# Kernel optimization log

Hardware: AMD Instinct MI355X
Metric: run time of the kernel (lower is better)

The kernel has to match this reference:

```python
import jax, jax.numpy as jnp
import numpy as np

EMB = 768
HEADS = 12
B, N = 32, 1024


def setup_inputs() -> dict:
    key = jax.random.key(0)
    ks = jax.random.split(key, 7)
    s = 1.0 / np.sqrt(EMB)
    return {
        "x": jax.random.normal(ks[0], (B, N, EMB), dtype=jnp.float32),
        "Wq": jax.random.normal(ks[1], (EMB, EMB), dtype=jnp.float32) * s,
        "bq": jnp.zeros((EMB,), dtype=jnp.float32),
        "Wk": jax.random.normal(ks[2], (EMB, EMB), dtype=jnp.float32) * s,
        "bk": jnp.zeros((EMB,), dtype=jnp.float32),
        "Wv": jax.random.normal(ks[3], (EMB, EMB), dtype=jnp.float32) * s,
        "bv": jnp.zeros((EMB,), dtype=jnp.float32),
    }


def reference(x, Wq, bq, Wk, bk, Wv, bv):
    b, n, _ = x.shape
    h = HEADS
    e = EMB // h  # head dim
    # project and split heads: b n (h e) -> b h n e
    def split(t):
        return t.reshape(b, n, h, e).transpose(0, 2, 1, 3)
    q = split(x @ Wq + bq)
    k = split(x @ Wk + bk)
    v = split(x @ Wv + bv)
    # NOTE: scale is 1/sqrt(num_head), as in the original module
    wei = jnp.einsum('bhie,bhje->bhij', q, k) / jnp.sqrt(jnp.float32(h))
    # NOTE: softmax over dim=2 = query axis i (non-standard)
    wei = jax.nn.softmax(wei, axis=2)
    # dropout is identity in eval mode
    out = jnp.einsum('bhij,bhje->bhie', wei, v)
    return out.transpose(0, 2, 1, 3).reshape(b, n, h * e)
```

## Files before the change

### kernel.cpp

```cpp
#include <hip/hip_runtime.h>

#define EMB 768
#define NH 12
#define HD 64
#define BB 32
#define NN 1024
#define QSCALE 0.41647025f

typedef _Float16 h8 __attribute__((ext_vector_type(8)));
typedef _Float16 h4 __attribute__((ext_vector_type(4)));
typedef _Float16 h2 __attribute__((ext_vector_type(2)));
typedef float f4 __attribute__((ext_vector_type(4)));

static __device__ __forceinline__ f4 mfma16(h8 a, h8 b, f4 c) {
  return __builtin_amdgcn_mfma_f32_16x16x32_f16(a, b, c, 0, 0, 0);
}

static __device__ __forceinline__ h2 cvt_pk(float a, float b) {
  return __builtin_bit_cast(h2, __builtin_amdgcn_cvt_pkrtz(a, b));
}

static __device__ __forceinline__ float exp2a(float x) {
#if __has_builtin(__builtin_amdgcn_exp2f)
  return __builtin_amdgcn_exp2f(x);
#else
  float r;
  asm("v_exp_f32 %0, %1\n\ts_nop 1" : "=v"(r) : "v"(x));
  return r;
#endif
}

__global__ __launch_bounds__(256) void k_cvt(const float* __restrict__ X,
                                             _Float16* __restrict__ Xh, int n4) {
  int i = blockIdx.x * 256 + threadIdx.x;
  if (i >= n4) return;
  float4 v = ((const float4*)X)[i];
  h4 o = {(_Float16)v.x, (_Float16)v.y, (_Float16)v.z, (_Float16)v.w};
  ((h4*)Xh)[i] = o;
}

__global__ __launch_bounds__(256) void k_wt(const float* __restrict__ W0,
                                            const float* __restrict__ W1,
                                            const float* __restrict__ W2,
                                            _Float16* __restrict__ Wt) {
  const float* W = blockIdx.z == 0 ? W0 : (blockIdx.z == 1 ? W1 : W2);
  _Float16* dst = Wt + (size_t)blockIdx.z * EMB * EMB;
  __shared__ float tile[64][65];
  const int t = threadIdx.x;
  const int r0 = blockIdx.y * 64, c0 = blockIdx.x * 64;
  const int r = t >> 4, c4 = (t & 15) * 4;
#pragma unroll
  for (int i = 0; i < 4; ++i) {
    const float4 v = *(const float4*)&W[(size_t)(r0 + r + 16 * i) * EMB + c0 + c4];
    tile[r + 16 * i][c4 + 0] = v.x; tile[r + 16 * i][c4 + 1] = v.y;
    tile[r + 16 * i][c4 + 2] = v.z; tile[r + 16 * i][c4 + 3] = v.w;
  }
  __syncthreads();
  const int cc = t >> 2, rr = (t & 3) * 16;
#pragma unroll
  for (int half = 0; half < 2; ++half) {
    h8 o;
#pragma unroll
    for (int j = 0; j < 8; ++j) o[j] = (_Float16)tile[rr + half * 8 + j][cc];
    *(h8*)&dst[(size_t)(c0 + cc) * EMB + r0 + rr + half * 8] = o;
  }
}

__global__ __launch_bounds__(256) void k_proj(const _Float16* __restrict__ Xh,
                                              const _Float16* __restrict__ Wt,
                                              const float* __restrict__ bias,
                                              _Float16* __restrict__ Out, float scale) {
  __shared__ _Float16 As[128][40];
  __shared__ _Float16 Bs[128][40];
  const int t = threadIdx.x;
  const int w = t >> 6, l = t & 63;
  const int wm = w >> 1, wn = w & 1;
  const int m0 = blockIdx.x * 128, n0 = blockIdx.y * 128;
  f4 acc[4][4];
#pragma unroll
  for (int mf = 0; mf < 4; ++mf)
#pragma unroll
    for (int nf = 0; nf < 4; ++nf) acc[mf][nf] = f4{0.f, 0.f, 0.f, 0.f};

  const int srow = t >> 2, sc = (t & 3) * 8;
  for (int k0 = 0; k0 < EMB; k0 += 32) {
#pragma unroll
    for (int i = 0; i < 2; ++i) {
      *(h8*)&As[srow + 64 * i][sc] = *(const h8*)&Xh[(size_t)(m0 + srow + 64 * i) * EMB + k0 + sc];
      *(h8*)&Bs[srow + 64 * i][sc] = *(const h8*)&Wt[(size_t)(n0 + srow + 64 * i) * EMB + k0 + sc];
    }
    __syncthreads();
    h8 af[4], bf[4];
#pragma unroll
    for (int mf = 0; mf < 4; ++mf) af[mf] = *(const h8*)&As[wm * 64 + mf * 16 + (l & 15)][(l >> 4) * 8];
#pragma unroll
    for (int nf = 0; nf < 4; ++nf) bf[nf] = *(const h8*)&Bs[wn * 64 + nf * 16 + (l & 15)][(l >> 4) * 8];
#pragma unroll
    for (int mf = 0; mf < 4; ++mf)
#pragma unroll
      for (int nf = 0; nf < 4; ++nf) acc[mf][nf] = mfma16(af[mf], bf[nf], acc[mf][nf]);
    __syncthreads();
  }
#pragma unroll
  for (int nf = 0; nf < 4; ++nf) {
    const int C = n0 + wn * 64 + nf * 16 + (l & 15);
    const float bvv = bias[C];
    const int h = C >> 6, e = C & 63;
#pragma unroll
    for (int mf = 0; mf < 4; ++mf) {
#pragma unroll
      for (int r = 0; r < 4; ++r) {
        const int R = m0 + wm * 64 + mf * 16 + (l >> 4) * 4 + r;
        const int b = R >> 10, tok = R & 1023;
        Out[((size_t)(b * NH + h) * NN + tok) * HD + e] = (_Float16)((acc[mf][nf][r] + bvv) * scale);
      }
    }
  }
}

__global__ __launch_bounds__(256) void k_stats(const _Float16* __restrict__ Q,
                                               const _Float16* __restrict__ K,
                                               float* __restrict__ Lg, float* __restrict__ MT) {
  const int bh = blockIdx.x * 48 + (blockIdx.y >> 3);
  const int jt = blockIdx.y & 7;
  const int j0 = jt * 128;
  __shared__ _Float16 Ks[128][64];
  __shared__ _Float16 Qs[128][64];
  __shared__ float Lj[128];
  __shared__ float reds[2][128];
  __shared__ float MsSh;
  const _Float16* Qb = Q + (size_t)bh * NN * HD;
  const _Float16* Kb = K + (size_t)bh * NN * HD;
  const int t = threadIdx.x, w = t >> 6, l = t & 63;
  const int wi = w >> 1, wj = w & 1;
  const int p = l & 15, g = l >> 4;
  const int lr = t >> 3, tc = t & 7;
  char* ksb = (char*)&Ks[0][0];
  char* qsb = (char*)&Qs[0][0];
#pragma unroll
  for (int i = 0; i < 4; ++i)
    *(h8*)(ksb + ((lr + 32 * i) << 7) + ((tc ^ (lr & 7)) << 4)) =
        *(const h8*)&Kb[(size_t)(j0 + lr + 32 * i) * HD + tc * 8];
  if (t < 128) Lj[t] = 0.f;
  __syncthreads();

  for (int i0 = 0; i0 < NN; i0 += 128) {
#pragma unroll
    for (int i = 0; i < 4; ++i)
      *(h8*)(qsb + ((lr + 32 * i) << 7) + ((tc ^ (lr & 7)) << 4)) =
          *(const h8*)&Qb[(size_t)(i0 + lr + 32 * i) * HD + tc * 8];
    __syncthreads();
    f4 s[4][4];
#pragma unroll
    for (int mf = 0; mf < 4; ++mf)
#pragma unroll
      for (int nf = 0; nf < 4; ++nf) s[mf][nf] = f4{0.f, 0.f, 0.f, 0.f};
#pragma unroll
    for (int ks = 0; ks < 2; ++ks) {
      h8 af[4], bf[4];
#pragma unroll
      for (int mf = 0; mf < 4; ++mf)
        af[mf] = *(const h8*)(qsb + ((wi * 64 + mf * 16 + p) << 7) + ((((ks << 2) | g) ^ (p & 7)) << 4));
#pragma unroll
      for (int nf = 0; nf < 4; ++nf)
        bf[nf] = *(const h8*)(ksb + ((wj * 64 + nf * 16 + p) << 7) + ((((ks << 2) | g) ^ (p & 7)) << 4));
#pragma unroll
      for (int mf = 0; mf < 4; ++mf)
#pragma unroll
        for (int nf = 0; nf < 4; ++nf) s[mf][nf] = mfma16(af[mf], bf[nf], s[mf][nf]);
    }
#pragma unroll
    for (int nf = 0; nf < 4; ++nf) {
      float cs = 0.f;
#pragma unroll
      for (int mf = 0; mf < 4; ++mf)
#pragma unroll
        for (int r = 0; r < 4; ++r) cs += exp2a(s[mf][nf][r]);
      cs += __shfl_xor(cs, 16);
      cs += __shfl_xor(cs, 32);
      if (l < 16) reds[wi][wj * 64 + nf * 16 + l] = cs;
    }
    __syncthreads();
    if (t < 128) Lj[t] += reds[0][t] + reds[1][t];
    __syncthreads();
  }
  if (w == 0) {
    float mv = fmaxf(Lj[l], Lj[l + 64]);
#pragma unroll
    for (int d = 32; d; d >>= 1) mv = fmaxf(mv, __shfl_xor(mv, d));
    if (l == 0) { MsSh = __log2f(mv); MT[bh * 8 + jt] = MsSh; }
  }
  __syncthreads();
  const float msc = exp2a(-MsSh);
  if (t < 128) Lg[(size_t)bh * NN + j0 + t] = Lj[t] * msc;
}

__global__ __launch_bounds__(256) void k_vt(const _Float16* __restrict__ Vtmp,
                                            const float* __restrict__ Lg,
                                            _Float16* __restrict__ Vt) {
  const int bh = blockIdx.y, j0 = blockIdx.x * 64;
  __shared__ _Float16 tile[64][72];
  const _Float16* src = Vtmp + (size_t)bh * NN * HD;
  _Float16* dst = Vt + (size_t)bh * HD * NN;
  const int t = threadIdx.x;
  const int jr = t >> 3, e8 = (t & 7) * 8;
#pragma unroll
  for (int i = 0; i < 2; ++i) {
    const float inv = 1.0f / Lg[(size_t)bh * NN + j0 + jr + 32 * i];
    h8 v = *(const h8*)&src[(size_t)(j0 + jr + 32 * i) * HD + e8];
    h8 o;
#pragma unroll
    for (int j = 0; j < 8; ++j) o[j] = (_Float16)((float)v[j] * inv);
    *(h8*)&tile[jr + 32 * i][e8] = o;
  }
  __syncthreads();
  const int er = t >> 3, j8 = (t & 7) * 8;
#pragma unroll
  for (int i = 0; i < 2; ++i) {
    h8 o;
#pragma unroll
    for (int j = 0; j < 8; ++j) o[j] = tile[j8 + j][er + 32 * i];
    *(h8*)&dst[(size_t)(er + 32 * i) * NN + j0 + j8] = o;
  }
}

__global__ __launch_bounds__(256) void k_out(const _Float16* __restrict__ Q,
                                             const _Float16* __restrict__ K,
                                             const _Float16* __restrict__ Vt,
                                             const float* __restrict__ MT,
                                             float* __restrict__ Out) {
  const int bh = blockIdx.x * 48 + (blockIdx.y >> 2);
  const int i0 = (blockIdx.y & 3) * 256;
  const int b = bh / NH, h = bh % NH;
  __shared__ _Float16 Ks[2][32][64];
  __shared__ _Float16 Vts[2][64][32];
  __shared__ _Float16 Ps[4][2][32][32];
  const _Float16* Qb = Q + (size_t)bh * NN * HD;
  const _Float16* Kb = K + (size_t)bh * NN * HD;
  const _Float16* Vb = Vt + (size_t)bh * HD * NN;
  const int t = threadIdx.x, w = t >> 6, l = t & 63;
  const int p = l & 15, g = l >> 4;
  char* psb[2] = {(char*)&Ps[w][0][0][0], (char*)&Ps[w][1][0][0]};

  h8 bq[2][2][2];
#pragma unroll
  for (int it = 0; it < 2; ++it)
#pragma unroll
    for (int f = 0; f < 2; ++f)
#pragma unroll
      for (int ks = 0; ks < 2; ++ks)
        bq[it][f][ks] = *(const h8*)&Qb[(size_t)(i0 + it * 128 + w * 32 + f * 16 + p) * HD + ks * 32 + g * 8];

  f4 oacc[2][4][2];
#pragma unroll
  for (int it = 0; it < 2; ++it)
#pragma unroll
    for (int ef = 0; ef < 4; ++ef)
#pragma unroll
      for (int f = 0; f < 2; ++f) oacc[it][ef][f] = f4{0.f, 0.f, 0.f, 0.f};

  const int kr = t >> 3, kc = t & 7;
  const int vr = t >> 2, vc = t & 3;

  h8 kreg = *(const h8*)&Kb[(size_t)kr * HD + kc * 8];
  h8 vreg = *(const h8*)&Vb[(size_t)vr * NN + vc * 8];
  *(h8*)((char*)&Ks[0][0][0] + (kr << 7) + ((kc ^ (kr & 7)) << 4)) = kreg;
  *(h8*)((char*)&Vts[0][0][0] + (vr << 6) + ((vc ^ ((vr >> 1) & 3)) << 4)) = vreg;

  for (int jt4 = 0; jt4 < 8; ++jt4) {
    const float Mstar = MT[bh * 8 + jt4];
#pragma unroll
    for (int u = 0; u < 4; ++u) {
      const int jt = jt4 * 4 + u;
      const int cur = u & 1;
      char* ksb = (char*)&Ks[cur][0][0];
      char* vsb = (char*)&Vts[cur][0][0];
      __syncthreads();
      if (jt + 1 < 32) {
        const int j0n = (jt + 1) * 32;
        kreg = *(const h8*)&Kb[(size_t)(j0n + kr) * HD + kc * 8];
        vreg = *(const h8*)&Vb[(size_t)vr * NN + j0n + vc * 8];
      }

      h8 ak[2][2], av[4];
#pragma unroll
      for (int ks = 0; ks < 2; ++ks)
#pragma unroll
        for (int jf = 0; jf < 2; ++jf)
          ak[ks][jf] = *(const h8*)(ksb + ((jf * 16 + p) << 7) + ((((ks << 2) | g) ^ (p & 7)) << 4));
#pragma unroll
      for (int ef = 0; ef < 4; ++ef)
        av[ef] = *(const h8*)(vsb + ((ef * 16 + p) << 6) + ((g ^ ((p >> 1) & 3)) << 4));

#pragma unroll
      for (int it = 0; it < 2; ++it) {
        f4 s[2][2];
#pragma unroll
        for (int f = 0; f < 2; ++f)
#pragma unroll
          for (int jf = 0; jf < 2; ++jf) s[f][jf] = f4{-Mstar, -Mstar, -Mstar, -Mstar};
#pragma unroll
        for (int ks = 0; ks < 2; ++ks)
#pragma unroll
          for (int f = 0; f < 2; ++f)
#pragma unroll
            for (int jf = 0; jf < 2; ++jf) s[f][jf] = mfma16(ak[ks][jf], bq[it][f][ks], s[f][jf]);
#pragma unroll
        for (int f = 0; f < 2; ++f)
#pragma unroll
          for (int jf = 0; jf < 2; ++jf) {
            const f4 sv = s[f][jf];
            h2 lo = cvt_pk(exp2a(sv[0]), exp2a(sv[1]));
            h2 hi = cvt_pk(exp2a(sv[2]), exp2a(sv[3]));
            h4 pw; pw[0] = lo[0]; pw[1] = lo[1]; pw[2] = hi[0]; pw[3] = hi[1];
            *(h4*)(psb[it] + ((f * 16 + p) << 6) +
                   (((2 * jf + (g >> 1)) ^ ((p >> 1) & 3)) << 4) + ((g & 1) << 3)) = pw;
          }
      }
      asm volatile("s_waitcnt lgkmcnt(0)" ::: "memory");
      __builtin_amdgcn_sched_barrier(0);

#pragma unroll
      for (int it = 0; it < 2; ++it) {
        h8 bp[2];
#pragma unroll
        for (int f = 0; f < 2; ++f)
          bp[f] = *(const h8*)(psb[it] + ((f * 16 + p) << 6) + ((g ^ ((p >> 1) & 3)) << 4));
#pragma unroll
        for (int ef = 0; ef < 4; ++ef)
#pragma unroll
          for (int f = 0; f < 2; ++f) oacc[it][ef][f] = mfma16(av[ef], bp[f], oacc[it][ef][f]);
      }

      if (jt + 1 < 32) {
        *(h8*)((char*)&Ks[cur ^ 1][0][0] + (kr << 7) + ((kc ^ (kr & 7)) << 4)) = kreg;
        *(h8*)((char*)&Vts[cur ^ 1][0][0] + (vr << 6) + ((vc ^ ((vr >> 1) & 3)) << 4)) = vreg;
      }
    }
  }

#pragma unroll
  for (int it = 0; it < 2; ++it) {
#pragma unroll
    for (int f = 0; f < 2; ++f) {
      const int i = i0 + it * 128 + w * 32 + f * 16 + p;
#pragma unroll
      for (int ef = 0; ef < 4; ++ef) {
        float4 o4 = {oacc[it][ef][f][0], oacc[it][ef][f][1], oacc[it][ef][f][2], oacc[it][ef][f][3]};
        *(float4*)&Out[((size_t)b * NN + i) * EMB + h * HD + ef * 16 + 4 * g] = o4;
      }
    }
  }
}

extern "C" void kernel_launch(void* const* d_in, const int* in_sizes, int n_in,
                              void* d_out, int out_size, void* d_ws, size_t ws_size,
                              hipStream_t stream) {
  const float* X  = (const float*)d_in[0];
  const float* Wq = (const float*)d_in[1];
  const float* bq = (const float*)d_in[2];
  const float* Wk = (const float*)d_in[3];
  const float* bk = (const float*)d_in[4];
  const float* Wv = (const float*)d_in[5];
  const float* bv = (const float*)d_in[6];

  char* ws = (char*)d_ws;
  _Float16* Qw = (_Float16*)(ws);
  _Float16* Kw = (_Float16*)(ws + 50331648);
  _Float16* Vt = (_Float16*)(ws + 100663296);
  _Float16* Wt = (_Float16*)(ws + 150994944);
  float* Lg    = (float*)(ws + 154533888);
  float* MT    = (float*)(ws + 156106752);

  _Float16* Xh   = (_Float16*)d_out;
  _Float16* Vtmp = (_Float16*)((char*)d_out + 50331648);
  float* Out = (float*)d_out;

  k_cvt<<<dim3(6291456 / 256), 256, 0, stream>>>(X, Xh, 6291456);
  k_wt<<<dim3(12, 12, 3), 256, 0, stream>>>(Wq, Wk, Wv, Wt);
  k_proj<<<dim3(256, 6), 256, 0, stream>>>(Xh, Wt,           bq, Qw,   QSCALE);
  k_proj<<<dim3(256, 6), 256, 0, stream>>>(Xh, Wt + 589824,  bk, Kw,   1.0f);
  k_proj<<<dim3(256, 6), 256, 0, stream>>>(Xh, Wt + 1179648, bv, Vtmp, 1.0f);
  k_stats<<<dim3(8, 384), 256, 0, stream>>>(Qw, Kw, Lg, MT);
  k_vt<<<dim3(16, 384), 256, 0, stream>>>(Vtmp, Lg, Vt);
  k_out<<<dim3(8, 192), 256, 0, stream>>>(Qw, Kw, Vt, MT, Out);
}
```

Baseline: 447.0 us.

## Fuse QKV projections into one GEMM with async LDS double-buffering

Replaces the three separate projection launches with one kernel over a 2304-wide concatenated weight, so each block picks its Q/K/V output, bias and scale from its column tile. K-tiles grow to 64 and are loaded straight into LDS with global_load_lds into a double buffer using an XOR swizzle. This is meant to overlap global loads with MFMA work, avoid LDS bank conflicts, cut launch overhead and improve X tile reuse through L2 across the fused N dimension. LDS use rises to 64KB per block, which may lower occupancy.

```diff
diff --git a/kernel.cpp b/kernel.cpp
--- a/kernel.cpp
+++ b/kernel.cpp
@@ -28,6 +28,12 @@
   asm("v_exp_f32 %0, %1\n\ts_nop 1" : "=v"(r) : "v"(x));
   return r;
 #endif
+}
+
+static __device__ __forceinline__ void gload16(const _Float16* g, _Float16* lds) {
+  __builtin_amdgcn_global_load_lds(
+      (const __attribute__((address_space(1))) void*)g,
+      (__attribute__((address_space(3))) void*)lds, 16, 0, 0);
 }
 
 __global__ __launch_bounds__(256) void k_cvt(const float* __restrict__ X,
@@ -66,53 +72,90 @@
   }
 }
 
-__global__ __launch_bounds__(256) void k_proj(const _Float16* __restrict__ Xh,
-                                              const _Float16* __restrict__ Wt,
-                                              const float* __restrict__ bias,
-                                              _Float16* __restrict__ Out, float scale) {
-  __shared__ _Float16 As[128][40];
-  __shared__ _Float16 Bs[128][40];
+__global__ __launch_bounds__(256) void k_projf(const _Float16* __restrict__ Xh,
+                                               const _Float16* __restrict__ Wt,
+                                               const float* __restrict__ bq,
+                                               const float* __restrict__ bk,
+                                               const float* __restrict__ bv,
+                                               _Float16* __restrict__ Qw,
+                                               _Float16* __restrict__ Kw,
+                                               _Float16* __restrict__ Vtmp) {
+  __shared__ _Float16 As[2][128 * 64];
+  __shared__ _Float16 Bs[2][128 * 64];
   const int t = threadIdx.x;
   const int w = t >> 6, l = t & 63;
   const int wm = w >> 1, wn = w & 1;
-  const int m0 = blockIdx.x * 128, n0 = blockIdx.y * 128;
+  const int p = l & 15, g = l >> 4;
+  const int by = blockIdx.x;
+  const int m0 = blockIdx.y * 128;
+  const int n0 = by * 128;
+
   f4 acc[4][4];
 #pragma unroll
   for (int mf = 0; mf < 4; ++mf)
 #pragma unroll
     for (int nf = 0; nf < 4; ++nf) acc[mf][nf] = f4{0.f, 0.f, 0.f, 0.f};
 
-  const int srow = t >> 2, sc = (t & 3) * 8;
-  for (int k0 = 0; k0 < EMB; k0 += 32) {
-#pragma unroll
-    for (int i = 0; i < 2; ++i) {
-      *(h8*)&As[srow + 64 * i][sc] = *(const h8*)&Xh[(size_t)(m0 + srow + 64 * i) * EMB + k0 + sc];
-      *(h8*)&Bs[srow + 64 * i][sc] = *(const h8*)&Wt[(size_t)(n0 + srow + 64 * i) * EMB + k0 + sc];
+  const int lrow = l >> 3, lch = (l & 7) ^ (l >> 3);
+
+#define STAGE(buf, k0)                                                            \
+  {                                                                               \
+    _Float16* ab = &As[buf][0];                                                   \
+    _Float16* bb = &Bs[buf][0];                                                   \
+    _Pragma("unroll") for (int i = 0; i < 4; ++i) {                               \
+      const int seg = (w << 2) | i;                                               \
+      const int grow = (seg << 3) | lrow;                                         \
+      gload16(Xh + (size_t)(m0 + grow) * EMB + (k0) + lch * 8, ab + seg * 512);   \
+      gload16(Wt + (size_t)(n0 + grow) * EMB + (k0) + lch * 8, bb + seg * 512);   \
+    }                                                                             \
+  }
+
+  STAGE(0, 0)
+  __syncthreads();
+
+  int cur = 0;
+  for (int kt = 0; kt < 12; ++kt) {
+    if (kt + 1 < 12) STAGE(cur ^ 1, (kt + 1) * 64)
+    const char* asb = (const char*)&As[cur][0];
+    const char* bsb = (const char*)&Bs[cur][0];
+#pragma unroll
+    for (int ks = 0; ks < 2; ++ks) {
+      h8 af[4], bf[4];
+#pragma unroll
+      for (int mf = 0; mf < 4; ++mf)
+        af[mf] = *(const h8*)(asb + ((wm * 64 + mf * 16 + p) << 7) +
+                              ((((ks << 2) | g) ^ (p & 7)) << 4));
+#pragma unroll
+      for (int nf = 0; nf < 4; ++nf)
+        bf[nf] = *(const h8*)(bsb + ((wn * 64 + nf * 16 + p) << 7) +
+                              ((((ks << 2) | g) ^ (p & 7)) << 4));
+#pragma unroll
+      for (int mf = 0; mf < 4; ++mf)
+#pragma unroll
+        for (int nf = 0; nf < 4; ++nf) acc[mf][nf] = mfma16(af[mf], bf[nf], acc[mf][nf]);
     }
     __syncthreads();
-    h8 af[4], bf[4];
-#pragma unroll
-    for (int mf = 0; mf < 4; ++mf) af[mf] = *(const h8*)&As[wm * 64 + mf * 16 + (l & 15)][(l >> 4) * 8];
-#pragma unroll
-    for (int nf = 0; nf < 4; ++nf) bf[nf] = *(const h8*)&Bs[wn * 64 + nf * 16 + (l & 15)][(l >> 4) * 8];
-#pragma unroll
-    for (int mf = 0; mf < 4; ++mf)
-#pragma unroll
-      for (int nf = 0; nf < 4; ++nf) acc[mf][nf] = mfma16(af[mf], bf[nf], acc[mf][nf]);
-    __syncthreads();
-  }
+    cur ^= 1;
+  }
+#undef STAGE
+
+  const int z = by / 6;
+  const int nl0 = (by % 6) * 128;
+  const float* bias = z == 0 ? bq : (z == 1 ? bk : bv);
+  _Float16* Outz = z == 0 ? Qw : (z == 1 ? Kw : Vtmp);
+  const float scale = z == 0 ? QSCALE : 1.0f;
 #pragma unroll
   for (int nf = 0; nf < 4; ++nf) {
-    const int C = n0 + wn * 64 + nf * 16 + (l & 15);
+    const int C = nl0 + wn * 64 + nf * 16 + p;
     const float bvv = bias[C];
     const int h = C >> 6, e = C & 63;
 #pragma unroll
     for (int mf = 0; mf < 4; ++mf) {
 #pragma unroll
       for (int r = 0; r < 4; ++r) {
-        const int R = m0 + wm * 64 + mf * 16 + (l >> 4) * 4 + r;
+        const int R = m0 + wm * 64 + mf * 16 + g * 4 + r;
         const int b = R >> 10, tok = R & 1023;
-        Out[((size_t)(b * NH + h) * NN + tok) * HD + e] = (_Float16)((acc[mf][nf][r] + bvv) * scale);
+        Outz[((size_t)(b * NH + h) * NN + tok) * HD + e] = (_Float16)((acc[mf][nf][r] + bvv) * scale);
       }
     }
   }
@@ -378,9 +421,7 @@
 
   k_cvt<<<dim3(6291456 / 256), 256, 0, stream>>>(X, Xh, 6291456);
   k_wt<<<dim3(12, 12, 3), 256, 0, stream>>>(Wq, Wk, Wv, Wt);
-  k_proj<<<dim3(256, 6), 256, 0, stream>>>(Xh, Wt,           bq, Qw,   QSCALE);
-  k_proj<<<dim3(256, 6), 256, 0, stream>>>(Xh, Wt + 589824,  bk, Kw,   1.0f);
-  k_proj<<<dim3(256, 6), 256, 0, stream>>>(Xh, Wt + 1179648, bv, Vtmp, 1.0f);
+  k_projf<<<dim3(18, 256), 256, 0, stream>>>(Xh, Wt, bq, bk, bv, Qw, Kw, Vtmp);
   k_stats<<<dim3(8, 384), 256, 0, stream>>>(Qw, Kw, Lg, MT);
   k_vt<<<dim3(16, 384), 256, 0, stream>>>(Vtmp, Lg, Vt);
   k_out<<<dim3(8, 192), 256, 0, stream>>>(Qw, Kw, Vt, MT, Out);
```

After: 397.3 us. -11.1%, faster.
